# Kernel tuning notes

Measured on AMD Instinct MI355X. Metric: run time of the kernel, lower is better.

The kernel has to match this reference:

```python
import jax, jax.numpy as jnp
import numpy as np

B, S, D, H = 2, 2048, 2048, 16
HD = D // H
WHERE_CONST = -10000.0

def setup_inputs() -> dict:
    key = jax.random.key(0)
    k1, k2, k3 = jax.random.split(key, 3)
    x = jax.random.normal(k1, (B, S, D), dtype=jnp.float32)
    attention_mask = jnp.zeros((B, 1, 1, S), dtype=jnp.float32)
    w_qkv = jax.random.normal(k2, (D, 3 * D), dtype=jnp.float32) * (1.0 / np.sqrt(D))
    b_qkv = jnp.zeros((3 * D,), dtype=jnp.float32)
    w_dense = jax.random.normal(k3, (D, D), dtype=jnp.float32) * (1.0 / np.sqrt(D))
    b_dense = jnp.zeros((D,), dtype=jnp.float32)
    return {"x": x, "attention_mask": attention_mask, "w_qkv": w_qkv,
            "b_qkv": b_qkv, "w_dense": w_dense, "b_dense": b_dense}

def reference(x, attention_mask, w_qkv, b_qkv, w_dense, b_dense):
    # fused QKV projection: [B,S,3D]
    qkv = jnp.einsum('bsd,de->bse', x, w_qkv) + b_qkv
    # [B,S,H,3*hd] -> [B,H,S,3*hd]
    qkv = qkv.reshape(B, S, H, 3 * HD).transpose(0, 2, 1, 3)
    q, k, v = jnp.split(qkv, 3, axis=-1)  # each [B,H,S,hd]
    # scores [B,H,S,S], scaled
    scores = jnp.einsum('bhqd,bhkd->bhqk', q, k) / np.sqrt(HD)
    causal = jnp.tril(jnp.ones((S, S), dtype=bool))[None, None]
    scores = jnp.where(causal, scores, WHERE_CONST)
    scores = scores + attention_mask
    probs = jax.nn.softmax(scores, axis=-1)
    # attention dropout is identity in eval mode
    ctx = jnp.einsum('bhqk,bhkd->bhqd', probs, v)  # [B,H,S,hd]
    ctx = ctx.transpose(0, 2, 1, 3).reshape(B, S, D)
    out = jnp.einsum('bsd,de->bse', ctx, w_dense) + b_dense
    # output dropout is identity in eval mode
    return out
```

## Files before the change

kernel.cpp:

```cpp
#include <hip/hip_runtime.h>
#include <hip/hip_bf16.h>

typedef __bf16 bf16x8 __attribute__((ext_vector_type(8)));
typedef float f32x4 __attribute__((ext_vector_type(4)));
typedef float f32x16 __attribute__((ext_vector_type(16)));
typedef unsigned short u16;

#define S_ 2048
#define D_ 2048
#define H_ 16
#define HD_ 128
#define SCALE_ 0.08838834764831845f

__device__ __forceinline__ u16 f2bf(float f) {
  unsigned u = __builtin_bit_cast(unsigned, f);
  u += 0x7fffu + ((u >> 16) & 1u);
  return (u16)(u >> 16);
}

__device__ __forceinline__ void gload16(void* lds, const void* g) {
  __builtin_amdgcn_global_load_lds((const __attribute__((address_space(1))) void*)g,
                                   (__attribute__((address_space(3))) void*)lds, 16, 0, 0);
}

__device__ __forceinline__ f32x4 mfma16(bf16x8 a, bf16x8 b, f32x4 c) {
  return __builtin_amdgcn_mfma_f32_16x16x32_bf16(a, b, c, 0, 0, 0);
}
__device__ __forceinline__ f32x16 mfma32(bf16x8 a, bf16x8 b, f32x16 c) {
  return __builtin_amdgcn_mfma_f32_32x32x16_bf16(a, b, c, 0, 0, 0);
}

__device__ __forceinline__ unsigned cvt_pk_bf16(float lo, float hi) {
  unsigned r;
  asm("v_cvt_pk_bf16_f32 %0, %1, %2" : "=v"(r) : "v"(lo), "v"(hi));
  return r;
}

__global__ void k_cast_bf16(const float* __restrict__ in, u16* __restrict__ out, int n4) {
  int i = blockIdx.x * blockDim.x + threadIdx.x;
  if (i < n4) {
    float4 v = ((const float4*)in)[i];
    ushort4 o;
    o.x = f2bf(v.x); o.y = f2bf(v.y); o.z = f2bf(v.z); o.w = f2bf(v.w);
    ((ushort4*)out)[i] = o;
  }
}

__global__ void k_transpose_cast(const float* __restrict__ in, u16* __restrict__ out,
                                 int rows, int cols) {
  __shared__ u16 tile[64][66];
  const int c0 = blockIdx.x * 64, r0 = blockIdx.y * 64;
  const int tx = threadIdx.x & 15, ty = threadIdx.x >> 4;
#pragma unroll
  for (int i = 0; i < 4; i++) {
    int r = ty + i * 16;
    float4 v = *(const float4*)&in[(long)(r0 + r) * cols + c0 + tx * 4];
    tile[r][tx * 4 + 0] = f2bf(v.x);
    tile[r][tx * 4 + 1] = f2bf(v.y);
    tile[r][tx * 4 + 2] = f2bf(v.z);
    tile[r][tx * 4 + 3] = f2bf(v.w);
  }
  __syncthreads();
#pragma unroll
  for (int i = 0; i < 4; i++) {
    int cc = ty + i * 16;
    ushort4 o;
    o.x = tile[tx * 4 + 0][cc];
    o.y = tile[tx * 4 + 1][cc];
    o.z = tile[tx * 4 + 2][cc];
    o.w = tile[tx * 4 + 3][cc];
    *(ushort4*)&out[(long)(c0 + cc) * rows + r0 + tx * 4] = o;
  }
}

__device__ __forceinline__ void qkv_store(u16* __restrict__ qb, u16* __restrict__ kpk,
                                          u16* __restrict__ vpk, int row, int col, float val) {
  u16 o = f2bf(val);
  int h = col / 384;
  int m3 = col - h * 384;
  int b = row >> 11, s = row & 2047;
  int bh = b * 16 + h, t = s >> 5;
  if (m3 < 128) {
    qb[(long)row * 2048 + h * 128 + m3] = o;
  } else if (m3 < 256) {
    int dd = m3 - 128;
    long idx = ((((long)bh * 64 + t) * 8 + (dd >> 4)) * 64 + (((dd >> 3) & 1) << 5) + (s & 31)) * 8 + (dd & 7);
    kpk[idx] = o;
  } else {
    int dd = m3 - 256;
    long idx = ((((long)bh * 64 + t) * 8 + (((s >> 4) & 1) << 2) + (dd >> 5)) * 64 + (((s >> 3) & 1) << 5) + (dd & 31)) * 8 + (s & 7);
    vpk[idx] = o;
  }
}

template <int MODE>
__global__ __launch_bounds__(256, 2) void k_gemm(const u16* __restrict__ A,
                                                 const u16* __restrict__ Bt,
                                                 const float* __restrict__ bias,
                                                 void* __restrict__ Cv,
                                                 int M, int N, int K, int NTM,
                                                 u16* __restrict__ qb,
                                                 u16* __restrict__ kpk,
                                                 u16* __restrict__ vpk) {
  __shared__ __align__(16) u16 lA[2][128 * 64];
  __shared__ __align__(16) u16 lB[2][128 * 64];
  const int tid = threadIdx.x, w = tid >> 6, l = tid & 63;
  const int wm = w >> 1, wn = w & 1, lr = l & 15, lg = l >> 4;
  const int nwg = NTM * (N >> 7);
  const int per = nwg >> 3;
  const int tnc = per / NTM;
  const int xcd = (int)blockIdx.x & 7;
  const int local = (int)blockIdx.x >> 3;
  const int ss = local / (8 * tnc), rr = local % (8 * tnc);
  const int tm = (ss * 8 + (rr & 7)) << 7;
  const int tn = (xcd * tnc + (rr >> 3)) << 7;
  const int NT = K >> 6;

  f32x4 acc[4][4];
#pragma unroll
  for (int m = 0; m < 4; m++)
#pragma unroll
    for (int n = 0; n < 4; n++) acc[m][n] = {0.f, 0.f, 0.f, 0.f};

  auto stageA = [&](int buf, int kt) {
#pragma unroll
    for (int i = 0; i < 4; i++) {
      int base = i * 256 + w * 64;
      int f = base + l, r = f >> 3, cg = (f & 7) ^ (r & 7);
      gload16(&lA[buf][base * 8], &A[(long)(tm + r) * K + kt * 64 + cg * 8]);
    }
  };
  auto stageB = [&](int buf, int kt) {
#pragma unroll
    for (int i = 0; i < 4; i++) {
      int base = i * 256 + w * 64;
      int f = base + l, r = f >> 3, cg = (f & 7) ^ (r & 7);
      gload16(&lB[buf][base * 8], &Bt[(long)(tn + r) * K + kt * 64 + cg * 8]);
    }
  };

  stageA(0, 0);
  stageB(0, 0);
  if (NT > 1) stageA(1, 1);
  asm volatile("s_waitcnt vmcnt(4)" ::: "memory");
  __builtin_amdgcn_s_barrier();

  for (int kt = 0; kt < NT; ++kt) {
    const int b = kt & 1;
    bf16x8 af[4][2], bfr[2][2];
#pragma unroll
    for (int m = 0; m < 4; m++)
#pragma unroll
      for (int k = 0; k < 2; k++) {
        int r = wm * 64 + m * 16 + lr;
        af[m][k] = *(const bf16x8*)&lA[b][r * 64 + ((((k << 2) + lg) ^ (r & 7)) << 3)];
      }
#pragma unroll
    for (int n = 0; n < 2; n++)
#pragma unroll
      for (int k = 0; k < 2; k++) {
        int r = wn * 64 + n * 16 + lr;
        bfr[n][k] = *(const bf16x8*)&lB[b][r * 64 + ((((k << 2) + lg) ^ (r & 7)) << 3)];
      }
    if (kt + 1 < NT) stageB(b ^ 1, kt + 1);
    __builtin_amdgcn_s_barrier();
    asm volatile("s_waitcnt lgkmcnt(0)" ::: "memory");
    __builtin_amdgcn_sched_barrier(0);
    __builtin_amdgcn_s_setprio(1);
#pragma unroll
    for (int m = 0; m < 4; m++)
#pragma unroll
      for (int n = 0; n < 2; n++)
#pragma unroll
        for (int k = 0; k < 2; k++)
          acc[m][n] = mfma16(af[m][k], bfr[n][k], acc[m][n]);
    __builtin_amdgcn_s_setprio(0);
    __builtin_amdgcn_s_barrier();

#pragma unroll
    for (int n = 0; n < 2; n++)
#pragma unroll
      for (int k = 0; k < 2; k++) {
        int r = wn * 64 + (n + 2) * 16 + lr;
        bfr[n][k] = *(const bf16x8*)&lB[b][r * 64 + ((((k << 2) + lg) ^ (r & 7)) << 3)];
      }
    if (kt + 2 < NT) stageA(b, kt + 2);
    __builtin_amdgcn_s_barrier();
    if (kt + 2 < NT)
      asm volatile("s_waitcnt vmcnt(4) lgkmcnt(0)" ::: "memory");
    else
      asm volatile("s_waitcnt vmcnt(0) lgkmcnt(0)" ::: "memory");
    __builtin_amdgcn_sched_barrier(0);
    __builtin_amdgcn_s_setprio(1);
#pragma unroll
    for (int m = 0; m < 4; m++)
#pragma unroll
      for (int n = 0; n < 2; n++)
#pragma unroll
        for (int k = 0; k < 2; k++)
          acc[m][n + 2] = mfma16(af[m][k], bfr[n][k], acc[m][n + 2]);
    __builtin_amdgcn_s_setprio(0);
    __builtin_amdgcn_s_barrier();
  }

#pragma unroll
  for (int n = 0; n < 4; n++) {
    int col = tn + wn * 64 + n * 16 + lr;
    float bv = bias[col];
#pragma unroll
    for (int m = 0; m < 4; m++) {
      int row0 = tm + wm * 64 + m * 16 + lg * 4;
#pragma unroll
      for (int j = 0; j < 4; j++) {
        float v = acc[m][n][j] + bv;
        if constexpr (MODE == 2)
          qkv_store(qb, kpk, vpk, row0 + j, col, v);
        else
          ((float*)Cv)[(long)(row0 + j) * N + col] = v;
      }
    }
  }
}

__global__ __launch_bounds__(256, 2) void k_attn(const u16* __restrict__ qb,
                                                 const u16* __restrict__ kpk,
                                                 const u16* __restrict__ vpk,
                                                 const float* __restrict__ amask,
                                                 u16* __restrict__ ctx) {
  const int bh = blockIdx.x, b = bh >> 4, h = bh & 15;
  const int tid = threadIdx.x, w = tid >> 6, l = tid & 63;
  const int lr5 = l & 31, hi = l >> 5;
  const int g = 15 - (int)blockIdx.y;
  const int c = 4 * g + w;

  const u16* kbase = kpk + (long)bh * 64 * 8 * 512 + l * 8;
  const u16* vbase = vpk + (long)bh * 64 * 8 * 512 + l * 8;
  const float* ab0 = amask + b * S_;

  const int qrow0 = c << 5;
  const int nt = c + 1;

  bf16x8 qf[8];
  {
    const u16* qp = qb + (long)(b * S_ + qrow0 + lr5) * 2048 + h * HD_ + hi * 8;
#pragma unroll
    for (int ks = 0; ks < 8; ks++) qf[ks] = *(const bf16x8*)(qp + ks * 16);
  }

  f32x16 aO[4];
#pragma unroll
  for (int db = 0; db < 4; db++)
#pragma unroll
    for (int r = 0; r < 16; r++) aO[db][r] = 0.f;
  float mrun = -3.0e38f, lrun = 0.f;

  bf16x8 kA[8], kB[8];
#pragma unroll
  for (int f = 0; f < 8; f++) kA[f] = *(const bf16x8*)(kbase + f * 512);

  auto body = [&](bf16x8 (&cur)[8], bf16x8 (&nxt)[8], int t) {
    const int t32 = t << 5;
    bf16x8 vf[8];
    {
      const u16* vp = vbase + (long)t * 4096;
#pragma unroll
      for (int f = 0; f < 8; f++) vf[f] = *(const bf16x8*)(vp + f * 512);
    }
    f32x4 am[4];
#pragma unroll
    for (int rg = 0; rg < 4; rg++) am[rg] = *(const f32x4*)(ab0 + t32 + rg * 8 + hi * 4);

    f32x16 aS;
#pragma unroll
    for (int r = 0; r < 16; r++) aS[r] = 0.f;
    __builtin_amdgcn_s_setprio(1);
#pragma unroll
    for (int ks = 0; ks < 8; ks++) aS = mfma32(cur[ks], qf[ks], aS);
    __builtin_amdgcn_s_setprio(0);

    if (t + 1 < nt) {
      const u16* kp = kbase + (long)(t + 1) * 4096;
#pragma unroll
      for (int f = 0; f < 8; f++) nxt[f] = *(const bf16x8*)(kp + f * 512);
    }

    float v[16];
    const bool needmask = (t == c);
#pragma unroll
    for (int rg = 0; rg < 4; rg++)
#pragma unroll
      for (int j = 0; j < 4; j++) {
        v[rg * 4 + j] = fmaf(aS[rg * 4 + j], SCALE_, am[rg][j]);
        if (needmask && (rg * 8 + hi * 4 + j > lr5)) v[rg * 4 + j] = -1e30f;
      }
    float mx = v[0];
#pragma unroll
    for (int i = 1; i < 16; i++) mx = fmaxf(mx, v[i]);
    mx = fmaxf(mx, __shfl_xor(mx, 32));

    if (!__all(mx <= mrun + 8.0f)) {
      float mnew = fmaxf(mrun, mx);
      float corr = __expf(mrun - mnew);
      lrun *= corr;
      mrun = mnew;
#pragma unroll
      for (int reg = 0; reg < 16; reg++) {
        float cb = __shfl(corr, (reg & 3) + 8 * (reg >> 2) + 4 * hi);
#pragma unroll
        for (int db = 0; db < 4; db++) aO[db][reg] *= cb;
      }
    }

    float ls = 0.f;
#pragma unroll
    for (int i = 0; i < 16; i++) { v[i] = __expf(v[i] - mrun); ls += v[i]; }
    ls += __shfl_xor(ls, 32);
    lrun += ls;

    unsigned pk[8];
#pragma unroll
    for (int q = 0; q < 8; q++) pk[q] = cvt_pk_bf16(v[2 * q], v[2 * q + 1]);
    bf16x8 pa[2];
#pragma unroll
    for (int kst = 0; kst < 2; kst++) {
      unsigned a0 = pk[4 * kst], a1 = pk[4 * kst + 1], a2 = pk[4 * kst + 2], a3 = pk[4 * kst + 3];
      unsigned s0 = hi ? a0 : a2;
      unsigned s1 = hi ? a1 : a3;
      unsigned r0 = __shfl_xor(s0, 32);
      unsigned r1 = __shfl_xor(s1, 32);
      union { unsigned u[4]; bf16x8 vv; } U;
      U.u[0] = hi ? r0 : a0;
      U.u[1] = hi ? r1 : a1;
      U.u[2] = hi ? a2 : r0;
      U.u[3] = hi ? a3 : r1;
      pa[kst] = U.vv;
    }

    __builtin_amdgcn_s_setprio(1);
#pragma unroll
    for (int kst = 0; kst < 2; kst++)
#pragma unroll
      for (int db = 0; db < 4; db++)
        aO[db] = mfma32(pa[kst], vf[kst * 4 + db], aO[db]);
    __builtin_amdgcn_s_setprio(0);
  };

  for (int t = 0; t < nt; t += 2) {
    body(kA, kB, t);
    if (t + 1 < nt) body(kB, kA, t + 1);
  }

  float inv = 1.0f / lrun;
#pragma unroll
  for (int reg = 0; reg < 16; reg++) {
    int r = (reg & 3) + 8 * (reg >> 2) + 4 * hi;
    float ib = __shfl(inv, r);
    int srow = qrow0 + r;
#pragma unroll
    for (int db = 0; db < 4; db++)
      ctx[(long)(b * S_ + srow) * D_ + h * HD_ + db * 32 + lr5] = f2bf(aO[db][reg] * ib);
  }
}

extern "C" void kernel_launch(void* const* d_in, const int* in_sizes, int n_in,
                              void* d_out, int out_size, void* d_ws, size_t ws_size,
                              hipStream_t stream) {
  const float* x  = (const float*)d_in[0];
  const float* am = (const float*)d_in[1];
  const float* wq = (const float*)d_in[2];
  const float* bq = (const float*)d_in[3];
  const float* wd = (const float*)d_in[4];
  const float* bd = (const float*)d_in[5];
  float* out = (float*)d_out;
  char* ws = (char*)d_ws;

  const size_t MB = 1048576;
  u16* xb   = (u16*)(ws);
  u16* wqT  = (u16*)(ws + 16 * MB);
  u16* qb   = (u16*)(ws + 40 * MB);
  u16* kpk  = (u16*)(ws + 56 * MB);
  u16* vpk  = (u16*)(ws + 72 * MB);
  u16* ctxb = (u16*)(ws);
  u16* wdT  = (u16*)(ws + 16 * MB);

  k_cast_bf16<<<8192, 256, 0, stream>>>(x, xb, 2097152);
  k_transpose_cast<<<dim3(96, 32), 256, 0, stream>>>(wq, wqT, 2048, 6144);
  k_gemm<2><<<1536, 256, 0, stream>>>(xb, wqT, bq, nullptr, 4096, 6144, 2048, 32, qb, kpk, vpk);
  k_transpose_cast<<<dim3(32, 32), 256, 0, stream>>>(wd, wdT, 2048, 2048);
  k_attn<<<dim3(32, 16), 256, 0, stream>>>(qb, kpk, vpk, am, ctxb);
  k_gemm<0><<<512, 256, 0, stream>>>(ctxb, wdT, bd, out, 4096, 2048, 2048, 32,
                                     nullptr, nullptr, nullptr);
}
```

Measured before the change: 259.0 us.

## Split attention KV range across waves and merge partial softmax in LDS

Each block now handles one 32-row query tile, and its four waves take interleaved KV tiles (stride 4) rather than each wave owning a separate query tile. The partial outputs, running maxima and sums go to shared memory and are merged with a log-sum-exp rescale, with each wave writing one 32-column slice. This gives a 4x larger grid and spreads the causal triangle's uneven work more evenly across waves. In exchange it adds about 70KB of LDS per block, which may cap occupancy, plus a barrier and a final merge.

```diff
diff --git a/kernel.cpp b/kernel.cpp
--- a/kernel.cpp
+++ b/kernel.cpp
@@ -227,19 +227,19 @@
                                                  const u16* __restrict__ vpk,
                                                  const float* __restrict__ amask,
                                                  u16* __restrict__ ctx) {
+  __shared__ float smO[4][64][65];
+  __shared__ float smM[4][32], smL[4][32];
   const int bh = blockIdx.x, b = bh >> 4, h = bh & 15;
   const int tid = threadIdx.x, w = tid >> 6, l = tid & 63;
   const int lr5 = l & 31, hi = l >> 5;
-  const int g = 15 - (int)blockIdx.y;
-  const int c = 4 * g + w;
+  const int c = 63 - (int)blockIdx.y;
+  const int qrow0 = c << 5;
+  const int nt = c + 1;
 
   const u16* kbase = kpk + (long)bh * 64 * 8 * 512 + l * 8;
   const u16* vbase = vpk + (long)bh * 64 * 8 * 512 + l * 8;
   const float* ab0 = amask + b * S_;
 
-  const int qrow0 = c << 5;
-  const int nt = c + 1;
-
   bf16x8 qf[8];
   {
     const u16* qp = qb + (long)(b * S_ + qrow0 + lr5) * 2048 + h * HD_ + hi * 8;
@@ -254,11 +254,16 @@
     for (int r = 0; r < 16; r++) aO[db][r] = 0.f;
   float mrun = -3.0e38f, lrun = 0.f;
 
+  const int cnt = (w <= c) ? ((nt - w + 3) >> 2) : 0;
+
   bf16x8 kA[8], kB[8];
-#pragma unroll
-  for (int f = 0; f < 8; f++) kA[f] = *(const bf16x8*)(kbase + f * 512);
-
-  auto body = [&](bf16x8 (&cur)[8], bf16x8 (&nxt)[8], int t) {
+  if (cnt) {
+    const u16* kp0 = kbase + (long)w * 4096;
+#pragma unroll
+    for (int f = 0; f < 8; f++) kA[f] = *(const bf16x8*)(kp0 + f * 512);
+  }
+
+  auto body = [&](bf16x8 (&cur)[8], bf16x8 (&nxt)[8], int t, bool pf) {
     const int t32 = t << 5;
     bf16x8 vf[8];
     {
@@ -278,8 +283,8 @@
     for (int ks = 0; ks < 8; ks++) aS = mfma32(cur[ks], qf[ks], aS);
     __builtin_amdgcn_s_setprio(0);
 
-    if (t + 1 < nt) {
-      const u16* kp = kbase + (long)(t + 1) * 4096;
+    if (pf) {
+      const u16* kp = kbase + (long)(t + 4) * 4096;
 #pragma unroll
       for (int f = 0; f < 8; f++) nxt[f] = *(const bf16x8*)(kp + f * 512);
     }
@@ -345,20 +350,33 @@
     __builtin_amdgcn_s_setprio(0);
   };
 
-  for (int t = 0; t < nt; t += 2) {
-    body(kA, kB, t);
-    if (t + 1 < nt) body(kB, kA, t + 1);
-  }
-
-  float inv = 1.0f / lrun;
-#pragma unroll
-  for (int reg = 0; reg < 16; reg++) {
-    int r = (reg & 3) + 8 * (reg >> 2) + 4 * hi;
-    float ib = __shfl(inv, r);
-    int srow = qrow0 + r;
-#pragma unroll
-    for (int db = 0; db < 4; db++)
-      ctx[(long)(b * S_ + srow) * D_ + h * HD_ + db * 32 + lr5] = f2bf(aO[db][reg] * ib);
+  for (int i = 0; i < cnt; i += 2) {
+    body(kA, kB, w + 4 * i, i + 1 < cnt);
+    if (i + 1 < cnt) body(kB, kA, w + 4 * (i + 1), i + 2 < cnt);
+  }
+
+#pragma unroll
+  for (int db = 0; db < 4; db++)
+#pragma unroll
+    for (int reg = 0; reg < 16; reg++) smO[w][l][db * 16 + reg] = aO[db][reg];
+  if (hi == 0) { smM[w][lr5] = mrun; smL[w][lr5] = lrun; }
+  __syncthreads();
+
+  {
+    const int db = w;
+#pragma unroll
+    for (int reg = 0; reg < 16; reg++) {
+      int r = (reg & 3) + 8 * (reg >> 2) + 4 * hi;
+      float m0 = smM[0][r], m1 = smM[1][r], m2 = smM[2][r], m3 = smM[3][r];
+      float ms = fmaxf(fmaxf(m0, m1), fmaxf(m2, m3));
+      float f0 = __expf(m0 - ms), f1 = __expf(m1 - ms);
+      float f2 = __expf(m2 - ms), f3 = __expf(m3 - ms);
+      float lsum = smL[0][r] * f0 + smL[1][r] * f1 + smL[2][r] * f2 + smL[3][r] * f3;
+      float val = smO[0][l][db * 16 + reg] * f0 + smO[1][l][db * 16 + reg] * f1 +
+                  smO[2][l][db * 16 + reg] * f2 + smO[3][l][db * 16 + reg] * f3;
+      int srow = qrow0 + r;
+      ctx[(long)(b * S_ + srow) * D_ + h * HD_ + db * 32 + lr5] = f2bf(val / lsum);
+    }
   }
 }
 
@@ -387,7 +405,7 @@
   k_transpose_cast<<<dim3(96, 32), 256, 0, stream>>>(wq, wqT, 2048, 6144);
   k_gemm<2><<<1536, 256, 0, stream>>>(xb, wqT, bq, nullptr, 4096, 6144, 2048, 32, qb, kpk, vpk);
   k_transpose_cast<<<dim3(32, 32), 256, 0, stream>>>(wd, wdT, 2048, 2048);
-  k_attn<<<dim3(32, 16), 256, 0, stream>>>(qb, kpk, vpk, am, ctxb);
+  k_attn<<<dim3(32, 64), 256, 0, stream>>>(qb, kpk, vpk, am, ctxb);
   k_gemm<0><<<512, 256, 0, stream>>>(ctxb, wdT, bd, out, 4096, 2048, 2048, 32,
                                      nullptr, nullptr, nullptr);
 }
```

New measurement: 258.0 us. About the same (-0.4%).
